# Optimization experiments

Measured on AMD Instinct MI355X. Metric: run time of the kernel, lower is better.

The kernel has to match this reference:

```python
import jax, jax.numpy as jnp
import numpy as np

B, T, I, H, V = 32, 64, 512, 512, 32000


def setup_inputs() -> dict:
    key = jax.random.key(0)
    ks = jax.random.split(key, 8)
    s_in = 1.0 / np.sqrt(H)  # torch LSTMCell/Linear uniform init scale
    return {
        "isequence": jax.random.normal(ks[0], (B, T, I), dtype=jnp.float32),
        "hidden_t": jax.random.normal(ks[1], (B, H), dtype=jnp.float32),
        "W_ih": jax.random.uniform(ks[2], (4 * H, I), jnp.float32, -s_in, s_in),
        "W_hh": jax.random.uniform(ks[3], (4 * H, H), jnp.float32, -s_in, s_in),
        "b_ih": jax.random.uniform(ks[4], (4 * H,), jnp.float32, -s_in, s_in),
        "b_hh": jax.random.uniform(ks[5], (4 * H,), jnp.float32, -s_in, s_in),
        "W_out": jax.random.uniform(ks[6], (V, H), jnp.float32, -s_in, s_in),
        "b_out": jax.random.uniform(ks[7], (V,), jnp.float32, -s_in, s_in),
    }


def reference(isequence, hidden_t, W_ih, W_hh, b_ih, b_hh, W_out, b_out):
    # isequence: [B, T, I] -> time-major [T, B, I] (matches permute(1,0,2))
    xs = jnp.transpose(isequence, (1, 0, 2))
    # Precompute input-to-gate projections for all timesteps: [T, B, 4H]
    x_gates = jnp.einsum("tbi,gi->tbg", xs, W_ih) + b_ih + b_hh
    c0 = jnp.zeros_like(hidden_t)  # init_hidden zeros cell state

    def step(carry, xg):
        h, c = carry
        gates = xg + h @ W_hh.T  # [B, 4H], torch gate order: i, f, g, o
        i_g, f_g, g_g, o_g = jnp.split(gates, 4, axis=-1)
        i_g = jax.nn.sigmoid(i_g)
        f_g = jax.nn.sigmoid(f_g)
        g_g = jnp.tanh(g_g)
        o_g = jax.nn.sigmoid(o_g)
        c_new = f_g * c + i_g * g_g
        h_new = o_g * jnp.tanh(c_new)
        logits = h_new @ W_out.T + b_out  # [B, V]
        return (h_new, c_new), logits

    _, osequence = jax.lax.scan(step, (hidden_t, c0), x_gates)  # [T, B, V]
    return jnp.transpose(osequence, (1, 0, 2))  # [B, T, V]
```

## Files before the change

### kernel.cpp

```cpp
#include <hip/hip_runtime.h>
#include <hip/hip_bf16.h>

typedef unsigned short u16;
typedef unsigned int u32;
typedef __attribute__((ext_vector_type(4))) float f32x4;
typedef __attribute__((ext_vector_type(8))) short short8;
typedef __attribute__((ext_vector_type(4))) unsigned short u16x4;
typedef __attribute__((ext_vector_type(4))) unsigned int u32x4;

#define LSTM_NBLK 16

static __device__ __forceinline__ u16 f2bf(float f) {
  union { float f; unsigned u; } v; v.f = f;
  unsigned r = v.u + 0x7FFFu + ((v.u >> 16) & 1u);
  return (u16)(r >> 16);
}

static __device__ __forceinline__ void gload_lds16(const void* g, void* l) {
  __builtin_amdgcn_global_load_lds(
      (const __attribute__((address_space(1))) unsigned int*)g,
      (__attribute__((address_space(3))) unsigned int*)l, 16, 0, 0);
}

static __device__ __forceinline__ short8 ld_b128_sc(const void* p) {
  short8 r;
  asm volatile("global_load_dwordx4 %0, %1, off sc0 sc1"
               : "=v"(r) : "v"(p) : "memory");
  return r;
}
static __device__ __forceinline__ unsigned ld_u32_sc_wait(const unsigned* p) {
  unsigned r;
  asm volatile("global_load_dword %0, %1, off sc0 sc1\n\ts_waitcnt vmcnt(0)"
               : "=v"(r) : "v"(p) : "memory");
  return r;
}
static __device__ __forceinline__ void st_u32_sc(void* p, unsigned v) {
  asm volatile("global_store_dword %0, %1, off sc0 sc1"
               :: "v"(p), "v"(v) : "memory");
}
static __device__ __forceinline__ void waitcnt0() {
  asm volatile("s_waitcnt vmcnt(0)" ::: "memory");
  __builtin_amdgcn_sched_barrier(0);
}

__global__ void prep_kernel(const float* __restrict__ iseq, const float* __restrict__ h0,
                            const float* __restrict__ wih, const float* __restrict__ whh,
                            const float* __restrict__ wout,
                            u16* __restrict__ wout_bf, u16* __restrict__ wih_bf,
                            u16* __restrict__ whh_bf, u16* __restrict__ ax,
                            u32* __restrict__ h2u, unsigned* __restrict__ flags) {
  const int S0 = 4096000;
  const int S1 = S0 + 262144;
  const int S2 = S1 + 262144;
  const int S3 = S2 + 262144;
  const int S4 = S3 + 8192;
  const int S5 = S4 + 4096;
  int u = blockIdx.x * blockDim.x + threadIdx.x;
  int stride = gridDim.x * blockDim.x;
  for (; u < S5; u += stride) {
    if (u < S0) {
      int e = u * 4; f32x4 v = *(const f32x4*)(wout + e);
      u16x4 o; o[0]=f2bf(v[0]); o[1]=f2bf(v[1]); o[2]=f2bf(v[2]); o[3]=f2bf(v[3]);
      *(u16x4*)(wout_bf + e) = o;
    } else if (u < S1) {
      int e = (u - S0) * 4; f32x4 v = *(const f32x4*)(wih + e);
      u16x4 o; o[0]=f2bf(v[0]); o[1]=f2bf(v[1]); o[2]=f2bf(v[2]); o[3]=f2bf(v[3]);
      *(u16x4*)(wih_bf + e) = o;
    } else if (u < S2) {
      int e = (u - S1) * 4; f32x4 v = *(const f32x4*)(whh + e);
      u16x4 o; o[0]=f2bf(v[0]); o[1]=f2bf(v[1]); o[2]=f2bf(v[2]); o[3]=f2bf(v[3]);
      *(u16x4*)(whh_bf + e) = o;
    } else if (u < S3) {
      int e = (u - S2) * 4; int m = e >> 9; int k = e & 511;
      int b = m & 31; int t = m >> 5;
      f32x4 v = *(const f32x4*)(iseq + ((b * 64 + t) << 9) + k);
      u16x4 o; o[0]=f2bf(v[0]); o[1]=f2bf(v[1]); o[2]=f2bf(v[2]); o[3]=f2bf(v[3]);
      *(u16x4*)(ax + e) = o;
    } else if (u < S4) {
      int v = u - S3;
      int e = v * 2;
      float lo = h0[e], hi = h0[e + 1];
      h2u[v] = (((u32)f2bf(hi)) << 16) | (u32)f2bf(lo);
    } else {
      flags[u - S4] = 0u;
    }
  }
}

__global__ __launch_bounds__(256, 2) void gemm_bt(
    const u16* __restrict__ A, const u16* __restrict__ Bw,
    float* __restrict__ C, const float* __restrict__ bias1,
    const float* __restrict__ bias2, int N, int remap) {
  __shared__ u16 As[2][8192];
  __shared__ u16 Bs[2][8192];
  const int tid = threadIdx.x;
  const int w = tid >> 6, l = tid & 63;
  const int wr = w >> 1, wc = w & 1;
  const int lid = blockIdx.x;
  const int cpx = gridDim.x >> 3;
  const int lid2 = (lid & 7) * cpx + (lid >> 3);
  const int tn = (lid2 >> 4) * 128;
  const int tm = (lid2 & 15) * 128;

  f32x4 acc[4][4];
#pragma unroll
  for (int i = 0; i < 4; ++i)
#pragma unroll
    for (int j = 0; j < 4; ++j) acc[i][j] = (f32x4){0.f, 0.f, 0.f, 0.f};

  auto stage = [&](int buf, int kt) {
#pragma unroll
    for (int i = 0; i < 4; ++i) {
      int r = (w * 4 + i) * 8 + (l >> 3);
      int c16 = (l & 7) ^ (r & 7);
      int rowm = tm + r;
      const u16* srca;
      if (remap) {
        srca = A + ((rowm & 63) + 1) * 16384 + (rowm >> 6) * 512 + kt * 64 + c16 * 8;
      } else {
        srca = A + rowm * 512 + kt * 64 + c16 * 8;
      }
      gload_lds16(srca, &As[buf][(w * 4 + i) * 512]);
      const u16* srcb = Bw + (tn + r) * 512 + kt * 64 + c16 * 8;
      gload_lds16(srcb, &Bs[buf][(w * 4 + i) * 512]);
    }
  };

  stage(0, 0);
  int buf = 0;
  for (int kt = 0; kt < 8; ++kt) {
    __syncthreads();
    if (kt < 7) stage(buf ^ 1, kt + 1);
#pragma unroll
    for (int kk = 0; kk < 2; ++kk) {
      short8 af[4], bfr[4];
#pragma unroll
      for (int mi = 0; mi < 4; ++mi) {
        int row = wr * 64 + mi * 16 + (l & 15);
        int s = (kk * 4 + (l >> 4)) ^ (row & 7);
        af[mi] = *(const short8*)&As[buf][row * 64 + s * 8];
      }
#pragma unroll
      for (int ni = 0; ni < 4; ++ni) {
        int row = wc * 64 + ni * 16 + (l & 15);
        int s = (kk * 4 + (l >> 4)) ^ (row & 7);
        bfr[ni] = *(const short8*)&Bs[buf][row * 64 + s * 8];
      }
#pragma unroll
      for (int mi = 0; mi < 4; ++mi)
#pragma unroll
        for (int ni = 0; ni < 4; ++ni)
          acc[mi][ni] = __builtin_amdgcn_mfma_f32_16x16x32_bf16(
              af[mi], bfr[ni], acc[mi][ni], 0, 0, 0);
    }
    buf ^= 1;
  }

#pragma unroll
  for (int ni = 0; ni < 4; ++ni) {
    int gcol = tn + wc * 64 + ni * 16 + (l & 15);
    float bv = 0.f;
    if (bias1) bv += bias1[gcol];
    if (bias2) bv += bias2[gcol];
#pragma unroll
    for (int mi = 0; mi < 4; ++mi) {
      int grow0 = tm + wr * 64 + mi * 16 + ((l >> 4) << 2);
      f32x4 a = acc[mi][ni];
#pragma unroll
      for (int q = 0; q < 4; ++q) {
        C[(long long)(grow0 + q) * N + gcol] = a[q] + bv;
      }
    }
  }
}

__global__ __launch_bounds__(512, 1) void lstm_persist(
    const u16* __restrict__ whh, const float* __restrict__ xg,
    u16* __restrict__ h2, unsigned* __restrict__ flags) {
  __shared__ u16 hbuf[32 * 512];
  __shared__ u16 hloc[1024];
  const int tid = threadIdx.x;
  const int w = tid >> 6, l = tid & 63;
  const int blk = blockIdx.x;
  const int j0 = (blk * 8 + w) * 4;
  const int c = l & 15;
  const int wrow = (c >> 2) * 512 + j0 + (c & 3);
  const int ko = (l >> 4) * 8;
  u32* h2u = (u32*)h2;

  short8 bfr[16];
  const u16* wp = whh + wrow * 512 + ko;
#pragma unroll
  for (int kt = 0; kt < 16; ++kt) bfr[kt] = *(const short8*)(wp + kt * 32);

  const int rq = (l >> 4) * 4;
  const int jj = l & 3;
  const int b0 = l & 15, b1 = 16 + (l & 15);
  const int s0 = b0 & 7;

  const int cb = tid & 31;
  const int ckg = tid >> 5;
  const int csw = cb & 7;

  const int ob = tid >> 4;
  const int oj = tid & 15;

  float creg[2][4];
#pragma unroll
  for (int mt = 0; mt < 2; ++mt)
#pragma unroll
    for (int q = 0; q < 4; ++q) creg[mt][q] = 0.f;

  float xcur[2][4], xnext[2][4];
#pragma unroll
  for (int mt = 0; mt < 2; ++mt)
#pragma unroll
    for (int q = 0; q < 4; ++q)
      xcur[mt][q] = xg[(mt * 16 + rq + q) * 2048 + wrow];

  for (int it = 0; it < 64; ++it) {
    if (it > 0 && w == 0) {
      const unsigned want = (unsigned)it;
      for (;;) {
        unsigned f = ld_u32_sc_wait(flags + blk * 256 + (l & 15) * 16);
        if (__all((int)(f >= want))) break;
      }
    }
    __syncthreads();

    {
      const u16* src = h2 + it * 16384 + cb * 512 + ckg * 32;
      short8 d0 = ld_b128_sc(src);
      short8 d1 = ld_b128_sc(src + 8);
      short8 d2 = ld_b128_sc(src + 16);
      short8 d3 = ld_b128_sc(src + 24);
      waitcnt0();
      *(short8*)&hbuf[cb * 512 + (((ckg * 4 + 0) ^ csw) * 8)] = d0;
      *(short8*)&hbuf[cb * 512 + (((ckg * 4 + 1) ^ csw) * 8)] = d1;
      *(short8*)&hbuf[cb * 512 + (((ckg * 4 + 2) ^ csw) * 8)] = d2;
      *(short8*)&hbuf[cb * 512 + (((ckg * 4 + 3) ^ csw) * 8)] = d3;
    }
    __syncthreads();

    f32x4 acc0 = (f32x4){0.f, 0.f, 0.f, 0.f};
    f32x4 acc1 = (f32x4){0.f, 0.f, 0.f, 0.f};
#pragma unroll
    for (int kt = 0; kt < 16; ++kt) {
      int x = ((kt * 4 + (l >> 4)) ^ s0) * 8;
      short8 a0 = *(const short8*)&hbuf[b0 * 512 + x];
      short8 a1 = *(const short8*)&hbuf[b1 * 512 + x];
      acc0 = __builtin_amdgcn_mfma_f32_16x16x32_bf16(a0, bfr[kt], acc0, 0, 0, 0);
      acc1 = __builtin_amdgcn_mfma_f32_16x16x32_bf16(a1, bfr[kt], acc1, 0, 0, 0);
    }
    if (it < 63) {
#pragma unroll
      for (int mt = 0; mt < 2; ++mt)
#pragma unroll
        for (int q = 0; q < 4; ++q)
          xnext[mt][q] = xg[((it + 1) * 32 + mt * 16 + rq + q) * 2048 + wrow];
    }

#pragma unroll
    for (int mt = 0; mt < 2; ++mt) {
#pragma unroll
      for (int q = 0; q < 4; ++q) {
        float av = (mt == 0) ? acc0[q] : acc1[q];
        float gp = av + xcur[mt][q];
        int bl = (l & 48) | jj;
        float xi = __shfl(gp, bl);
        float xf = __shfl(gp, bl | 4);
        float xgg = __shfl(gp, bl | 8);
        float xo = __shfl(gp, bl | 12);
        float is = 1.f / (1.f + __expf(-xi));
        float fs = 1.f / (1.f + __expf(-xf));
        float e2 = __expf(2.f * xgg);
        float gt = 1.f - 2.f / (e2 + 1.f);
        float os = 1.f / (1.f + __expf(-xo));
        float cn = fs * creg[mt][q] + is * gt;
        creg[mt][q] = cn;
        float e2c = __expf(2.f * cn);
        float hn = os * (1.f - 2.f / (e2c + 1.f));
        if ((l & 12) == 0) {
          int b = mt * 16 + rq + q;
          hloc[b * 32 + w * 4 + jj] = f2bf(hn);
        }
      }
    }
    __syncthreads();

    {
      u32 v = *(const u32*)&hloc[ob * 32 + oj * 2];
      st_u32_sc(h2u + (it + 1) * 8192 + ob * 256 + blk * 16 + oj, v);
      waitcnt0();
    }
    __syncthreads();

    if (it < 63) {
      if (w == 0 && l < 16)
        st_u32_sc(flags + l * 256 + blk * 16, (unsigned)(it + 1));
#pragma unroll
      for (int mt = 0; mt < 2; ++mt)
#pragma unroll
        for (int q = 0; q < 4; ++q)
          xcur[mt][q] = xnext[mt][q];
    }
  }
}

extern "C" void kernel_launch(void* const* d_in, const int* in_sizes, int n_in,
                              void* d_out, int out_size, void* d_ws, size_t ws_size,
                              hipStream_t stream) {
  (void)in_sizes; (void)n_in; (void)out_size; (void)ws_size;
  const float* iseq = (const float*)d_in[0];
  const float* h0   = (const float*)d_in[1];
  const float* wih  = (const float*)d_in[2];
  const float* whh  = (const float*)d_in[3];
  const float* bih  = (const float*)d_in[4];
  const float* bhh  = (const float*)d_in[5];
  const float* wout = (const float*)d_in[6];
  const float* bout = (const float*)d_in[7];

  char* ws = (char*)d_ws;
  u16* wout_bf = (u16*)(ws + 0);
  u16* wih_bf  = (u16*)(ws + 32768000);
  u16* whh_bf  = (u16*)(ws + 34865152);
  u16* ax      = (u16*)(ws + 36962304);
  u16* h2      = (u16*)(ws + 39059456);
  unsigned* flags = (unsigned*)(ws + 41189376);
  float* xg    = (float*)(ws + 41254912);
  float* out   = (float*)d_out;

  prep_kernel<<<4096, 256, 0, stream>>>(iseq, h0, wih, whh, wout,
                                        wout_bf, wih_bf, whh_bf, ax,
                                        (u32*)h2, flags);
  gemm_bt<<<256, 256, 0, stream>>>(ax, wih_bf, xg, bih, bhh, 2048, 0);
  lstm_persist<<<LSTM_NBLK, 512, 0, stream>>>(whh_bf, xg, h2, flags);
  gemm_bt<<<4000, 256, 0, stream>>>(h2, wout_bf, out, bout, nullptr, 32000, 1);
}
```

Before: 560.2 us.

## Fuse input projection into persistent LSTM and overlap W_out conversion

```diff
diff --git a/kernel.cpp b/kernel.cpp
--- a/kernel.cpp
+++ b/kernel.cpp
@@ -9,6 +9,7 @@
 typedef __attribute__((ext_vector_type(4))) unsigned int u32x4;
 
 #define LSTM_NBLK 16
+#define LSTM_GRID 240
 
 static __device__ __forceinline__ u16 f2bf(float f) {
   union { float f; unsigned u; } v; v.f = f;
@@ -45,42 +46,44 @@
 
 __global__ void prep_kernel(const float* __restrict__ iseq, const float* __restrict__ h0,
                             const float* __restrict__ wih, const float* __restrict__ whh,
-                            const float* __restrict__ wout,
-                            u16* __restrict__ wout_bf, u16* __restrict__ wih_bf,
-                            u16* __restrict__ whh_bf, u16* __restrict__ ax,
-                            u32* __restrict__ h2u, unsigned* __restrict__ flags) {
-  const int S0 = 4096000;
+                            const float* __restrict__ bih, const float* __restrict__ bhh,
+                            u16* __restrict__ wih_bf, u16* __restrict__ whh_bf,
+                            u16* __restrict__ ax, u32* __restrict__ h2u,
+                            float* __restrict__ bsum, unsigned* __restrict__ flags) {
+  const int S0 = 262144;
   const int S1 = S0 + 262144;
   const int S2 = S1 + 262144;
-  const int S3 = S2 + 262144;
-  const int S4 = S3 + 8192;
+  const int S3 = S2 + 8192;
+  const int S4 = S3 + 512;
   const int S5 = S4 + 4096;
   int u = blockIdx.x * blockDim.x + threadIdx.x;
   int stride = gridDim.x * blockDim.x;
   for (; u < S5; u += stride) {
     if (u < S0) {
-      int e = u * 4; f32x4 v = *(const f32x4*)(wout + e);
-      u16x4 o; o[0]=f2bf(v[0]); o[1]=f2bf(v[1]); o[2]=f2bf(v[2]); o[3]=f2bf(v[3]);
-      *(u16x4*)(wout_bf + e) = o;
-    } else if (u < S1) {
-      int e = (u - S0) * 4; f32x4 v = *(const f32x4*)(wih + e);
+      int e = u * 4; f32x4 v = *(const f32x4*)(wih + e);
       u16x4 o; o[0]=f2bf(v[0]); o[1]=f2bf(v[1]); o[2]=f2bf(v[2]); o[3]=f2bf(v[3]);
       *(u16x4*)(wih_bf + e) = o;
-    } else if (u < S2) {
-      int e = (u - S1) * 4; f32x4 v = *(const f32x4*)(whh + e);
+    } else if (u < S1) {
+      int e = (u - S0) * 4; f32x4 v = *(const f32x4*)(whh + e);
       u16x4 o; o[0]=f2bf(v[0]); o[1]=f2bf(v[1]); o[2]=f2bf(v[2]); o[3]=f2bf(v[3]);
       *(u16x4*)(whh_bf + e) = o;
-    } else if (u < S3) {
-      int e = (u - S2) * 4; int m = e >> 9; int k = e & 511;
+    } else if (u < S2) {
+      int e = (u - S1) * 4; int m = e >> 9; int k = e & 511;
       int b = m & 31; int t = m >> 5;
       f32x4 v = *(const f32x4*)(iseq + ((b * 64 + t) << 9) + k);
       u16x4 o; o[0]=f2bf(v[0]); o[1]=f2bf(v[1]); o[2]=f2bf(v[2]); o[3]=f2bf(v[3]);
       *(u16x4*)(ax + e) = o;
-    } else if (u < S4) {
-      int v = u - S3;
+    } else if (u < S3) {
+      int v = u - S2;
       int e = v * 2;
       float lo = h0[e], hi = h0[e + 1];
       h2u[v] = (((u32)f2bf(hi)) << 16) | (u32)f2bf(lo);
+    } else if (u < S4) {
+      int e = (u - S3) * 4;
+      f32x4 a = *(const f32x4*)(bih + e);
+      f32x4 b4 = *(const f32x4*)(bhh + e);
+      f32x4 s; s[0]=a[0]+b4[0]; s[1]=a[1]+b4[1]; s[2]=a[2]+b4[2]; s[3]=a[3]+b4[3];
+      *(f32x4*)(bsum + e) = s;
     } else {
       flags[u - S4] = 0u;
     }
@@ -89,8 +92,7 @@
 
 __global__ __launch_bounds__(256, 2) void gemm_bt(
     const u16* __restrict__ A, const u16* __restrict__ Bw,
-    float* __restrict__ C, const float* __restrict__ bias1,
-    const float* __restrict__ bias2, int N, int remap) {
+    float* __restrict__ C, const float* __restrict__ bias1, int N) {
   __shared__ u16 As[2][8192];
   __shared__ u16 Bs[2][8192];
   const int tid = threadIdx.x;
@@ -114,12 +116,7 @@
       int r = (w * 4 + i) * 8 + (l >> 3);
       int c16 = (l & 7) ^ (r & 7);
       int rowm = tm + r;
-      const u16* srca;
-      if (remap) {
-        srca = A + ((rowm & 63) + 1) * 16384 + (rowm >> 6) * 512 + kt * 64 + c16 * 8;
-      } else {
-        srca = A + rowm * 512 + kt * 64 + c16 * 8;
-      }
+      const u16* srca = A + ((rowm & 63) + 1) * 16384 + (rowm >> 6) * 512 + kt * 64 + c16 * 8;
       gload_lds16(srca, &As[buf][(w * 4 + i) * 512]);
       const u16* srcb = Bw + (tn + r) * 512 + kt * 64 + c16 * 8;
       gload_lds16(srcb, &Bs[buf][(w * 4 + i) * 512]);
@@ -159,9 +156,7 @@
 #pragma unroll
   for (int ni = 0; ni < 4; ++ni) {
     int gcol = tn + wc * 64 + ni * 16 + (l & 15);
-    float bv = 0.f;
-    if (bias1) bv += bias1[gcol];
-    if (bias2) bv += bias2[gcol];
+    float bv = bias1 ? bias1[gcol] : 0.f;
 #pragma unroll
     for (int mi = 0; mi < 4; ++mi) {
       int grow0 = tm + wr * 64 + mi * 16 + ((l >> 4) << 2);
@@ -175,11 +170,25 @@
 }
 
 __global__ __launch_bounds__(512, 1) void lstm_persist(
-    const u16* __restrict__ whh, const float* __restrict__ xg,
-    u16* __restrict__ h2, unsigned* __restrict__ flags) {
+    const u16* __restrict__ whh, const u16* __restrict__ wih,
+    const u16* __restrict__ ax, const float* __restrict__ bsum,
+    u16* __restrict__ h2, unsigned* __restrict__ flags,
+    const float* __restrict__ wout, u16* __restrict__ wout_bf) {
   __shared__ u16 hbuf[32 * 512];
   __shared__ u16 hloc[1024];
   const int tid = threadIdx.x;
+
+  if (blockIdx.x >= LSTM_NBLK) {
+    int idx = (blockIdx.x - LSTM_NBLK) * 512 + tid;
+    int stride = (LSTM_GRID - LSTM_NBLK) * 512;
+    for (int u2 = idx; u2 < 4096000; u2 += stride) {
+      int e = u2 * 4; f32x4 v = *(const f32x4*)(wout + e);
+      u16x4 o; o[0]=f2bf(v[0]); o[1]=f2bf(v[1]); o[2]=f2bf(v[2]); o[3]=f2bf(v[3]);
+      *(u16x4*)(wout_bf + e) = o;
+    }
+    return;
+  }
+
   const int w = tid >> 6, l = tid & 63;
   const int blk = blockIdx.x;
   const int j0 = (blk * 8 + w) * 4;
@@ -188,10 +197,17 @@
   const int ko = (l >> 4) * 8;
   u32* h2u = (u32*)h2;
 
-  short8 bfr[16];
-  const u16* wp = whh + wrow * 512 + ko;
-#pragma unroll
-  for (int kt = 0; kt < 16; ++kt) bfr[kt] = *(const short8*)(wp + kt * 32);
+  short8 bfr[16], bfi[16];
+  {
+    const u16* wp = whh + wrow * 512 + ko;
+    const u16* wpi = wih + wrow * 512 + ko;
+#pragma unroll
+    for (int kt = 0; kt < 16; ++kt) {
+      bfr[kt] = *(const short8*)(wp + kt * 32);
+      bfi[kt] = *(const short8*)(wpi + kt * 32);
+    }
+  }
+  const float bsr = bsum[wrow];
 
   const int rq = (l >> 4) * 4;
   const int jj = l & 3;
@@ -212,11 +228,21 @@
     for (int q = 0; q < 4; ++q) creg[mt][q] = 0.f;
 
   float xcur[2][4], xnext[2][4];
-#pragma unroll
-  for (int mt = 0; mt < 2; ++mt)
-#pragma unroll
-    for (int q = 0; q < 4; ++q)
-      xcur[mt][q] = xg[(mt * 16 + rq + q) * 2048 + wrow];
+  {
+    f32x4 xa0 = (f32x4){bsr, bsr, bsr, bsr};
+    f32x4 xa1 = xa0;
+    const u16* pa0 = ax + b0 * 512 + ko;
+    const u16* pa1 = ax + b1 * 512 + ko;
+#pragma unroll
+    for (int kt = 0; kt < 16; ++kt) {
+      short8 a0 = *(const short8*)(pa0 + kt * 32);
+      short8 a1 = *(const short8*)(pa1 + kt * 32);
+      xa0 = __builtin_amdgcn_mfma_f32_16x16x32_bf16(a0, bfi[kt], xa0, 0, 0, 0);
+      xa1 = __builtin_amdgcn_mfma_f32_16x16x32_bf16(a1, bfi[kt], xa1, 0, 0, 0);
+    }
+#pragma unroll
+    for (int q = 0; q < 4; ++q) { xcur[0][q] = xa0[q]; xcur[1][q] = xa1[q]; }
+  }
 
   for (int it = 0; it < 64; ++it) {
     if (it > 0 && w == 0) {
@@ -252,12 +278,21 @@
       acc0 = __builtin_amdgcn_mfma_f32_16x16x32_bf16(a0, bfr[kt], acc0, 0, 0, 0);
       acc1 = __builtin_amdgcn_mfma_f32_16x16x32_bf16(a1, bfr[kt], acc1, 0, 0, 0);
     }
+
     if (it < 63) {
-#pragma unroll
-      for (int mt = 0; mt < 2; ++mt)
-#pragma unroll
-        for (int q = 0; q < 4; ++q)
-          xnext[mt][q] = xg[((it + 1) * 32 + mt * 16 + rq + q) * 2048 + wrow];
+      f32x4 xa0 = (f32x4){bsr, bsr, bsr, bsr};
+      f32x4 xa1 = xa0;
+      const u16* pa0 = ax + ((it + 1) * 32 + b0) * 512 + ko;
+      const u16* pa1 = ax + ((it + 1) * 32 + b1) * 512 + ko;
+#pragma unroll
+      for (int kt = 0; kt < 16; ++kt) {
+        short8 a0 = *(const short8*)(pa0 + kt * 32);
+        short8 a1 = *(const short8*)(pa1 + kt * 32);
+        xa0 = __builtin_amdgcn_mfma_f32_16x16x32_bf16(a0, bfi[kt], xa0, 0, 0, 0);
+        xa1 = __builtin_amdgcn_mfma_f32_16x16x32_bf16(a1, bfi[kt], xa1, 0, 0, 0);
+      }
+#pragma unroll
+      for (int q = 0; q < 4; ++q) { xnext[0][q] = xa0[q]; xnext[1][q] = xa1[q]; }
     }
 
 #pragma unroll
@@ -327,13 +362,13 @@
   u16* ax      = (u16*)(ws + 36962304);
   u16* h2      = (u16*)(ws + 39059456);
   unsigned* flags = (unsigned*)(ws + 41189376);
-  float* xg    = (float*)(ws + 41254912);
+  float* bsum  = (float*)(ws + 41205760);
   float* out   = (float*)d_out;
 
-  prep_kernel<<<4096, 256, 0, stream>>>(iseq, h0, wih, whh, wout,
-                                        wout_bf, wih_bf, whh_bf, ax,
-                                        (u32*)h2, flags);
-  gemm_bt<<<256, 256, 0, stream>>>(ax, wih_bf, xg, bih, bhh, 2048, 0);
-  lstm_persist<<<LSTM_NBLK, 512, 0, stream>>>(whh_bf, xg, h2, flags);
-  gemm_bt<<<4000, 256, 0, stream>>>(h2, wout_bf, out, bout, nullptr, 32000, 1);
-}
+  prep_kernel<<<2048, 256, 0, stream>>>(iseq, h0, wih, whh, bih, bhh,
+                                        wih_bf, whh_bf, ax, (u32*)h2,
+                                        bsum, flags);
+  lstm_persist<<<LSTM_GRID, 512, 0, stream>>>(whh_bf, wih_bf, ax, bsum,
+                                              h2, flags, wout, wout_bf);
+  gemm_bt<<<4000, 256, 0, stream>>>(h2, wout_bf, out, bout, 32000);
+}
```

Result: slower. 949.2 us (+69.4%).

## Overlap W_out bf16 conversion with persistent LSTM recurrence using idle blocks

Applied to the files above, without the earlier changes.

```diff
diff --git a/kernel.cpp b/kernel.cpp
--- a/kernel.cpp
+++ b/kernel.cpp
@@ -9,6 +9,7 @@
 typedef __attribute__((ext_vector_type(4))) unsigned int u32x4;
 
 #define LSTM_NBLK 16
+#define LSTM_GRID 240
 
 static __device__ __forceinline__ u16 f2bf(float f) {
   union { float f; unsigned u; } v; v.f = f;
@@ -45,44 +46,38 @@
 
 __global__ void prep_kernel(const float* __restrict__ iseq, const float* __restrict__ h0,
                             const float* __restrict__ wih, const float* __restrict__ whh,
-                            const float* __restrict__ wout,
-                            u16* __restrict__ wout_bf, u16* __restrict__ wih_bf,
-                            u16* __restrict__ whh_bf, u16* __restrict__ ax,
-                            u32* __restrict__ h2u, unsigned* __restrict__ flags) {
-  const int S0 = 4096000;
+                            u16* __restrict__ wih_bf, u16* __restrict__ whh_bf,
+                            u16* __restrict__ ax, u32* __restrict__ h2u,
+                            unsigned* __restrict__ flags) {
+  const int S0 = 262144;
   const int S1 = S0 + 262144;
   const int S2 = S1 + 262144;
-  const int S3 = S2 + 262144;
-  const int S4 = S3 + 8192;
-  const int S5 = S4 + 4096;
+  const int S3 = S2 + 8192;
+  const int S4 = S3 + 4096;
   int u = blockIdx.x * blockDim.x + threadIdx.x;
   int stride = gridDim.x * blockDim.x;
-  for (; u < S5; u += stride) {
+  for (; u < S4; u += stride) {
     if (u < S0) {
-      int e = u * 4; f32x4 v = *(const f32x4*)(wout + e);
-      u16x4 o; o[0]=f2bf(v[0]); o[1]=f2bf(v[1]); o[2]=f2bf(v[2]); o[3]=f2bf(v[3]);
-      *(u16x4*)(wout_bf + e) = o;
-    } else if (u < S1) {
-      int e = (u - S0) * 4; f32x4 v = *(const f32x4*)(wih + e);
+      int e = u * 4; f32x4 v = *(const f32x4*)(wih + e);
       u16x4 o; o[0]=f2bf(v[0]); o[1]=f2bf(v[1]); o[2]=f2bf(v[2]); o[3]=f2bf(v[3]);
       *(u16x4*)(wih_bf + e) = o;
-    } else if (u < S2) {
-      int e = (u - S1) * 4; f32x4 v = *(const f32x4*)(whh + e);
+    } else if (u < S1) {
+      int e = (u - S0) * 4; f32x4 v = *(const f32x4*)(whh + e);
       u16x4 o; o[0]=f2bf(v[0]); o[1]=f2bf(v[1]); o[2]=f2bf(v[2]); o[3]=f2bf(v[3]);
       *(u16x4*)(whh_bf + e) = o;
-    } else if (u < S3) {
-      int e = (u - S2) * 4; int m = e >> 9; int k = e & 511;
+    } else if (u < S2) {
+      int e = (u - S1) * 4; int m = e >> 9; int k = e & 511;
       int b = m & 31; int t = m >> 5;
       f32x4 v = *(const f32x4*)(iseq + ((b * 64 + t) << 9) + k);
       u16x4 o; o[0]=f2bf(v[0]); o[1]=f2bf(v[1]); o[2]=f2bf(v[2]); o[3]=f2bf(v[3]);
       *(u16x4*)(ax + e) = o;
-    } else if (u < S4) {
-      int v = u - S3;
+    } else if (u < S3) {
+      int v = u - S2;
       int e = v * 2;
       float lo = h0[e], hi = h0[e + 1];
       h2u[v] = (((u32)f2bf(hi)) << 16) | (u32)f2bf(lo);
     } else {
-      flags[u - S4] = 0u;
+      flags[u - S3] = 0u;
     }
   }
 }
@@ -176,10 +171,23 @@
 
 __global__ __launch_bounds__(512, 1) void lstm_persist(
     const u16* __restrict__ whh, const float* __restrict__ xg,
-    u16* __restrict__ h2, unsigned* __restrict__ flags) {
+    u16* __restrict__ h2, unsigned* __restrict__ flags,
+    const float* __restrict__ wout, u16* __restrict__ wout_bf) {
   __shared__ u16 hbuf[32 * 512];
   __shared__ u16 hloc[1024];
   const int tid = threadIdx.x;
+
+  if (blockIdx.x >= LSTM_NBLK) {
+    int idx = (blockIdx.x - LSTM_NBLK) * 512 + tid;
+    int stride = (LSTM_GRID - LSTM_NBLK) * 512;
+    for (int u2 = idx; u2 < 4096000; u2 += stride) {
+      int e = u2 * 4; f32x4 v = *(const f32x4*)(wout + e);
+      u16x4 o; o[0]=f2bf(v[0]); o[1]=f2bf(v[1]); o[2]=f2bf(v[2]); o[3]=f2bf(v[3]);
+      *(u16x4*)(wout_bf + e) = o;
+    }
+    return;
+  }
+
   const int w = tid >> 6, l = tid & 63;
   const int blk = blockIdx.x;
   const int j0 = (blk * 8 + w) * 4;
@@ -330,10 +338,10 @@
   float* xg    = (float*)(ws + 41254912);
   float* out   = (float*)d_out;
 
-  prep_kernel<<<4096, 256, 0, stream>>>(iseq, h0, wih, whh, wout,
-                                        wout_bf, wih_bf, whh_bf, ax,
-                                        (u32*)h2, flags);
+  prep_kernel<<<2048, 256, 0, stream>>>(iseq, h0, wih, whh,
+                                        wih_bf, whh_bf, ax, (u32*)h2, flags);
   gemm_bt<<<256, 256, 0, stream>>>(ax, wih_bf, xg, bih, bhh, 2048, 0);
-  lstm_persist<<<LSTM_NBLK, 512, 0, stream>>>(whh_bf, xg, h2, flags);
+  lstm_persist<<<LSTM_GRID, 512, 0, stream>>>(whh_bf, xg, h2, flags,
+                                              wout, wout_bf);
   gemm_bt<<<4000, 256, 0, stream>>>(h2, wout_bf, out, bout, nullptr, 32000, 1);
 }
```

After: 546.0 us. 1.03x faster.
